# Kernel tuning notes

Hardware: AMD Instinct MI355X
Metric: run time of the kernel (lower is better)

Reference implementation:

```python
import jax, jax.numpy as jnp
import numpy as np

N_NODES = 50000
N_HYPEREDGES = 50000
E = 320000
D = 256


def _prelu(x, a):
    return jnp.where(x >= 0, x, a * x)


def _hypergraph_conv(x, hei, W, b, num_nodes, num_edges):
    # PyG HypergraphConv, use_attention=False, heads=1:
    # out = D^{-1} H B^{-1} H^T (X W^T) + b
    src = hei[0]  # node indices, [E]
    he = hei[1]   # hyperedge indices, [E]
    xw = x @ W.T  # [N, D] node transform (lin has no bias)
    ones = jnp.ones((hei.shape[1],), x.dtype)
    deg_n = jax.ops.segment_sum(ones, src, num_segments=num_nodes)   # node degree D
    deg_e = jax.ops.segment_sum(ones, he, num_segments=num_edges)    # hyperedge size B
    d_inv = jnp.where(deg_n > 0, 1.0 / deg_n, 0.0)
    b_inv = jnp.where(deg_e > 0, 1.0 / deg_e, 0.0)
    # node -> hyperedge aggregation, scaled by B^{-1}
    edge_feat = b_inv[:, None] * jax.ops.segment_sum(xw[src], he, num_segments=num_edges)  # [n_he, D]
    # hyperedge -> node aggregation, scaled by D^{-1}
    out = d_inv[:, None] * jax.ops.segment_sum(edge_feat[he], src, num_segments=num_nodes)  # [N, D]
    return out + b


def setup_inputs() -> dict:
    key = jax.random.key(0)
    ks = jax.random.split(key, 6)
    std = np.sqrt(2.0 / D)  # kaiming_normal
    x = jax.random.normal(ks[0], (N_NODES, D), dtype=jnp.float32)
    hyper_edge_index = jax.random.randint(ks[1], (2, E), 0, N_HYPEREDGES, dtype=jnp.int64)
    W1 = jax.random.normal(ks[2], (D, D), dtype=jnp.float32) * std
    b1 = jnp.zeros((D,), jnp.float32)
    W2 = jax.random.normal(ks[3], (D, D), dtype=jnp.float32) * std
    b2 = jnp.zeros((D,), jnp.float32)
    prelu_a = jnp.asarray(0.25, jnp.float32)
    return {"x": x, "W1": W1, "b1": b1, "W2": W2, "b2": b2,
            "prelu_a": prelu_a, "hyper_edge_index": hyper_edge_index}


def reference(x, W1, b1, W2, b2, prelu_a, hyper_edge_index):
    out = _hypergraph_conv(x, hyper_edge_index, W1, b1, N_NODES, N_HYPEREDGES)
    out = _prelu(out, prelu_a)
    out = _hypergraph_conv(out, hyper_edge_index, W2, b2, N_NODES, N_HYPEREDGES)
    out = out + x  # residual
    out = _prelu(out, prelu_a)
    return out
```

## Files before the change

kernel.cpp:

```cpp
#include <hip/hip_runtime.h>

#define NN    50000
#define NHE   50000
#define NEDGE 320000
#define DD    256

#define SB    1024
#define NBLK  ((NN + SB - 1) / SB)
#define CNTB  ((NEDGE / 4 + 255) / 256)

typedef float f32x4 __attribute__((ext_vector_type(4)));
typedef short short8 __attribute__((ext_vector_type(8)));

static __device__ __forceinline__ unsigned short f2b(float f) {
    union { float f; unsigned u; } c; c.f = f;
    unsigned u = c.u;
    u += 0x7fffu + ((u >> 16) & 1u);
    return (unsigned short)(u >> 16);
}
static __device__ __forceinline__ float b2f_lo(unsigned v) {
    union { unsigned u; float f; } c; c.u = v << 16; return c.f;
}
static __device__ __forceinline__ float b2f_hi(unsigned v) {
    union { unsigned u; float f; } c; c.u = v & 0xffff0000u; return c.f;
}
static __device__ __forceinline__ unsigned pack2(float a, float b) {
    return (unsigned)f2b(a) | ((unsigned)f2b(b) << 16);
}

static __device__ __forceinline__ void glds16(const unsigned short* g, unsigned short* l) {
    __builtin_amdgcn_global_load_lds((const __attribute__((address_space(1))) unsigned int*)g,
                                     (__attribute__((address_space(3))) unsigned int*)l,
                                     16, 0, 0);
}

__global__ __launch_bounds__(256) void k_count_cvt(const int* __restrict__ src,
                                                   const int* __restrict__ he,
                                                   int* __restrict__ cnt_n,
                                                   int* __restrict__ cnt_e,
                                                   int* __restrict__ rank_n,
                                                   int* __restrict__ rank_e,
                                                   const float* __restrict__ w1,
                                                   const float* __restrict__ w2,
                                                   unsigned short* __restrict__ o1,
                                                   unsigned short* __restrict__ o2) {
    int bx = blockIdx.x;
    if (bx >= CNTB) {
        int t = (bx - CNTB) * 256 + threadIdx.x;
        const int n4 = DD * DD / 4;
        const float* s = (t < n4) ? w1 : w2;
        unsigned short* d = (t < n4) ? o1 : o2;
        int i = (t < n4) ? t : t - n4;
        float4 v = ((const float4*)s)[i];
        uint2 o;
        o.x = pack2(v.x, v.y);
        o.y = pack2(v.z, v.w);
        ((uint2*)d)[i] = o;
        return;
    }
    int t  = bx * 256 + threadIdx.x;
    int e0 = t * 4;
    if (e0 >= NEDGE) return;
    int4 s = *(const int4*)(src + e0);
    int4 h = *(const int4*)(he + e0);
    int4 rn, re;
    rn.x = atomicAdd(&cnt_n[s.x], 1);
    rn.y = atomicAdd(&cnt_n[s.y], 1);
    rn.z = atomicAdd(&cnt_n[s.z], 1);
    rn.w = atomicAdd(&cnt_n[s.w], 1);
    re.x = atomicAdd(&cnt_e[h.x], 1);
    re.y = atomicAdd(&cnt_e[h.y], 1);
    re.z = atomicAdd(&cnt_e[h.z], 1);
    re.w = atomicAdd(&cnt_e[h.w], 1);
    *(int4*)(rank_n + e0) = rn;
    *(int4*)(rank_e + e0) = re;
}

__global__ __launch_bounds__(256) void k_scan_a(const int* __restrict__ cnt_n,
                                                const int* __restrict__ cnt_e,
                                                int* __restrict__ bsum) {
    int b   = blockIdx.x;
    int seg = b / NBLK, lb = b % NBLK;
    const int* cnt = seg ? cnt_e : cnt_n;
    int t = threadIdx.x;
    int idx = lb * SB + t * 4;
    int s = 0;
#pragma unroll
    for (int j = 0; j < 4; ++j)
        if (idx + j < NN) s += cnt[idx + j];
    __shared__ int red[256];
    red[t] = s;
    __syncthreads();
    for (int o = 128; o > 0; o >>= 1) {
        if (t < o) red[t] += red[t + o];
        __syncthreads();
    }
    if (t == 0) bsum[b] = red[0];
}

__global__ __launch_bounds__(256) void k_scan_c(const int* __restrict__ cnt_n,
                                                const int* __restrict__ cnt_e,
                                                const int* __restrict__ bsum,
                                                int* __restrict__ off_n,
                                                int* __restrict__ off_e) {
    int b   = blockIdx.x;
    int seg = b / NBLK, lb = b % NBLK;
    const int* cnt = seg ? cnt_e : cnt_n;
    int* off = seg ? off_e : off_n;
    int t = threadIdx.x;
    __shared__ int sb[NBLK];
    __shared__ int binfo[2];
    if (t < NBLK) sb[t] = bsum[seg * NBLK + t];
    __syncthreads();
    if (t == 0) {
        int base = 0, tot = 0;
        for (int j = 0; j < NBLK; ++j) { if (j < lb) base += sb[j]; tot += sb[j]; }
        binfo[0] = base; binfo[1] = tot;
    }
    int idx = lb * SB + t * 4;
    int v[4];
    int tsum = 0;
#pragma unroll
    for (int j = 0; j < 4; ++j) {
        v[j] = (idx + j < NN) ? cnt[idx + j] : 0;
        tsum += v[j];
    }
    __shared__ int sc[256];
    sc[t] = tsum;
    __syncthreads();
    for (int o = 1; o < 256; o <<= 1) {
        int val = (t >= o) ? sc[t - o] : 0;
        __syncthreads();
        sc[t] += val;
        __syncthreads();
    }
    int p = binfo[0] + sc[t] - tsum;
#pragma unroll
    for (int j = 0; j < 4; ++j) {
        if (idx + j < NN) off[idx + j] = p;
        p += v[j];
    }
    if (b == 0 && t == 0) off_n[NN] = binfo[1];
    if (b == NBLK && t == 0) off_e[NHE] = binfo[1];
}

__global__ __launch_bounds__(256) void k_fill(const int* __restrict__ src,
                                              const int* __restrict__ he,
                                              const int* __restrict__ off_n,
                                              const int* __restrict__ off_e,
                                              const int* __restrict__ rank_n,
                                              const int* __restrict__ rank_e,
                                              int* __restrict__ adj_n,
                                              int* __restrict__ adj_e) {
    int t  = blockIdx.x * 256 + threadIdx.x;
    int e0 = t * 4;
    if (e0 >= NEDGE) return;
    int4 s  = *(const int4*)(src + e0);
    int4 h  = *(const int4*)(he + e0);
    int4 rn = *(const int4*)(rank_n + e0);
    int4 re = *(const int4*)(rank_e + e0);
    int on0 = off_n[s.x], on1 = off_n[s.y], on2 = off_n[s.z], on3 = off_n[s.w];
    int oe0 = off_e[h.x], oe1 = off_e[h.y], oe2 = off_e[h.z], oe3 = off_e[h.w];
    adj_n[on0 + rn.x] = h.x;
    adj_n[on1 + rn.y] = h.y;
    adj_n[on2 + rn.z] = h.z;
    adj_n[on3 + rn.w] = h.w;
    adj_e[oe0 + re.x] = s.x;
    adj_e[oe1 + re.y] = s.y;
    adj_e[oe2 + re.z] = s.z;
    adj_e[oe3 + re.w] = s.w;
}

template <bool A32>
__global__ __launch_bounds__(1024) void k_gemm_bres(const void* __restrict__ Av,
                                                    const unsigned short* __restrict__ Wb,
                                                    unsigned short* __restrict__ Cb) {
    __shared__ __align__(16) unsigned short Bs[128 * 256];
    const int t    = threadIdx.x;
    const int lane = t & 63;
    const int wave = t >> 6;
    const int n0   = blockIdx.x * 128;

#pragma unroll
    for (int q = 0; q < 4; ++q) {
        int row   = q * 32 + wave * 2 + (lane >> 5);
        int chunk = lane & 31;
        glds16(Wb + (size_t)(n0 + row) * DD + ((chunk ^ (row & 7)) * 8),
               Bs + q * 8192 + wave * 512);
    }
    __syncthreads();

    const int fr = lane & 15;
    const int fq = lane >> 4;
    int chunk = blockIdx.y * 16 + wave;
    if (chunk * 16 >= NN) return;
    int m0 = chunk * 16;

    f32x4 acc[8] = {};
    short8 af[8];
    if (A32) {
        const float* p = (const float*)Av + (size_t)(m0 + fr) * DD + fq * 8;
#pragma unroll
        for (int kc = 0; kc < 8; ++kc) {
            const float* pp = p + kc * 32;
            float4 f0 = ((const float4*)pp)[0];
            float4 f1 = ((const float4*)pp)[1];
            uint4 u;
            u.x = pack2(f0.x, f0.y); u.y = pack2(f0.z, f0.w);
            u.z = pack2(f1.x, f1.y); u.w = pack2(f1.z, f1.w);
            af[kc] = *(short8*)&u;
        }
    } else {
        const unsigned short* p = (const unsigned short*)Av + (size_t)(m0 + fr) * DD + fq * 8;
#pragma unroll
        for (int kc = 0; kc < 8; ++kc)
            af[kc] = *(const short8*)(p + kc * 32);
    }

#pragma unroll
    for (int kc = 0; kc < 8; ++kc) {
#pragma unroll
        for (int nt = 0; nt < 8; ++nt) {
            int r  = nt * 16 + fr;
            int ch = (kc * 4 + fq) ^ (fr & 7);
            short8 bf = *(const short8*)(Bs + r * 256 + ch * 8);
            acc[nt] = __builtin_amdgcn_mfma_f32_16x16x32_bf16(af[kc], bf, acc[nt], 0, 0, 0);
        }
    }

#pragma unroll
    for (int nt = 0; nt < 8; ++nt)
#pragma unroll
        for (int i = 0; i < 4; ++i)
            Cb[(size_t)(m0 + fq * 4 + i) * DD + n0 + nt * 16 + fr] = f2b(acc[nt][i]);
}

static __device__ __forceinline__ void acc8(float* a, uint4 v) {
    a[0] += b2f_lo(v.x); a[1] += b2f_hi(v.x);
    a[2] += b2f_lo(v.y); a[3] += b2f_hi(v.y);
    a[4] += b2f_lo(v.z); a[5] += b2f_hi(v.z);
    a[6] += b2f_lo(v.w); a[7] += b2f_hi(v.w);
}
static __device__ __forceinline__ void gather8(const unsigned short* __restrict__ srcb,
                                               const int* __restrict__ adj,
                                               int b, int e, int sl, float* a) {
#pragma unroll
    for (int i = 0; i < 8; ++i) a[i] = 0.f;
    for (int i = b; i < e; i += 8) {
        int g0 = adj[i];
        int g[8];
        g[0] = g0;
#pragma unroll
        for (int j = 1; j < 8; ++j) g[j] = (i + j < e) ? adj[i + j] : g0;
        uint4 v[8];
#pragma unroll
        for (int j = 0; j < 8; ++j)
            v[j] = *(const uint4*)(srcb + (size_t)g[j] * DD + sl * 8);
        acc8(a, v[0]);
#pragma unroll
        for (int j = 1; j < 8; ++j)
            if (i + j < e) acc8(a, v[j]);
    }
}

__global__ __launch_bounds__(256) void k_gather_edge_b(const unsigned short* __restrict__ xw,
                                                       unsigned short* __restrict__ ef,
                                                       const int* __restrict__ off,
                                                       const int* __restrict__ adj) {
    int tid = blockIdx.x * 256 + threadIdx.x;
    int w = tid >> 5;
    int sl = tid & 31;
    if (w >= NHE) return;
    int b = off[w], e = off[w + 1];
    float a[8];
    gather8(xw, adj, b, e, sl, a);
    float sc = (e > b) ? 1.f / (float)(e - b) : 0.f;
    uint4 o;
    o.x = pack2(a[0] * sc, a[1] * sc);
    o.y = pack2(a[2] * sc, a[3] * sc);
    o.z = pack2(a[4] * sc, a[5] * sc);
    o.w = pack2(a[6] * sc, a[7] * sc);
    *(uint4*)(ef + (size_t)w * DD + sl * 8) = o;
}

__global__ __launch_bounds__(256) void k_gather_node_mid_b(const unsigned short* __restrict__ ef,
                                                           unsigned short* __restrict__ h,
                                                           const int* __restrict__ off,
                                                           const int* __restrict__ adj,
                                                           const float* __restrict__ bias,
                                                           const float* __restrict__ aP) {
    int tid = blockIdx.x * 256 + threadIdx.x;
    int w = tid >> 5;
    int sl = tid & 31;
    if (w >= NN) return;
    int b = off[w], e = off[w + 1];
    float a[8];
    gather8(ef, adj, b, e, sl, a);
    float sc = (e > b) ? 1.f / (float)(e - b) : 0.f;
    float al = *aP;
    float4 bb0 = ((const float4*)bias)[sl * 2];
    float4 bb1 = ((const float4*)bias)[sl * 2 + 1];
    float r[8];
    r[0] = a[0] * sc + bb0.x; r[1] = a[1] * sc + bb0.y;
    r[2] = a[2] * sc + bb0.z; r[3] = a[3] * sc + bb0.w;
    r[4] = a[4] * sc + bb1.x; r[5] = a[5] * sc + bb1.y;
    r[6] = a[6] * sc + bb1.z; r[7] = a[7] * sc + bb1.w;
#pragma unroll
    for (int i = 0; i < 8; ++i) r[i] = (r[i] >= 0.f) ? r[i] : al * r[i];
    uint4 o;
    o.x = pack2(r[0], r[1]);
    o.y = pack2(r[2], r[3]);
    o.z = pack2(r[4], r[5]);
    o.w = pack2(r[6], r[7]);
    *(uint4*)(h + (size_t)w * DD + sl * 8) = o;
}

__global__ __launch_bounds__(256) void k_gather_node_final_b(const unsigned short* __restrict__ ef,
                                                             const float* __restrict__ x,
                                                             float* __restrict__ out,
                                                             const int* __restrict__ off,
                                                             const int* __restrict__ adj,
                                                             const float* __restrict__ bias,
                                                             const float* __restrict__ aP) {
    int tid = blockIdx.x * 256 + threadIdx.x;
    int w = tid >> 5;
    int sl = tid & 31;
    if (w >= NN) return;
    int b = off[w], e = off[w + 1];
    float a[8];
    gather8(ef, adj, b, e, sl, a);
    float sc = (e > b) ? 1.f / (float)(e - b) : 0.f;
    float al = *aP;
    float4 bb0 = ((const float4*)bias)[sl * 2];
    float4 bb1 = ((const float4*)bias)[sl * 2 + 1];
    const float* xp = x + (size_t)w * DD + sl * 8;
    float4 xv0 = *(const float4*)xp;
    float4 xv1 = *(const float4*)(xp + 4);
    float r[8];
    r[0] = a[0] * sc + bb0.x + xv0.x; r[1] = a[1] * sc + bb0.y + xv0.y;
    r[2] = a[2] * sc + bb0.z + xv0.z; r[3] = a[3] * sc + bb0.w + xv0.w;
    r[4] = a[4] * sc + bb1.x + xv1.x; r[5] = a[5] * sc + bb1.y + xv1.y;
    r[6] = a[6] * sc + bb1.z + xv1.z; r[7] = a[7] * sc + bb1.w + xv1.w;
#pragma unroll
    for (int i = 0; i < 8; ++i) r[i] = (r[i] >= 0.f) ? r[i] : al * r[i];
    float* op = out + (size_t)w * DD + sl * 8;
    *(float4*)op = make_float4(r[0], r[1], r[2], r[3]);
    *(float4*)(op + 4) = make_float4(r[4], r[5], r[6], r[7]);
}

extern "C" void kernel_launch(void* const* d_in, const int* in_sizes, int n_in,
                              void* d_out, int out_size, void* d_ws, size_t ws_size,
                              hipStream_t stream) {
    const float* x       = (const float*)d_in[0];
    const float* W1      = (const float*)d_in[1];
    const float* b1      = (const float*)d_in[2];
    const float* W2      = (const float*)d_in[3];
    const float* b2      = (const float*)d_in[4];
    const float* prelu_a = (const float*)d_in[5];
    const int*   hei     = (const int*)d_in[6];
    const int* idx_src = hei;
    const int* idx_he  = hei + NEDGE;

    float* out = (float*)d_out;
    unsigned short* B1 = (unsigned short*)d_ws;
    unsigned short* B2 = B1 + (size_t)NN * DD;
    int* off_n  = (int*)(B2 + (size_t)NN * DD);
    int* off_e  = off_n + NN + 1;
    int* cnt_n  = off_e + NHE + 1;
    int* cnt_e  = cnt_n + NN;
    int* adj_n  = cnt_e + NHE;
    int* adj_e  = adj_n + NEDGE;
    int* rank_n = adj_e + NEDGE;
    int* rank_e = rank_n + NEDGE;
    int* bsum   = rank_e + NEDGE;
    unsigned short* w1b = (unsigned short*)d_out;
    unsigned short* w2b = w1b + DD * DD;

    const int gblocks = (NN * 32 + 255) / 256;
    dim3 ggrid(2, (NN / 16 + 15) / 16);

    hipMemsetAsync(cnt_n, 0, sizeof(int) * (NN + NHE), stream);
    k_count_cvt<<<CNTB + 128, 256, 0, stream>>>(idx_src, idx_he, cnt_n, cnt_e,
                                                rank_n, rank_e, W1, W2, w1b, w2b);
    k_scan_a<<<2 * NBLK, 256, 0, stream>>>(cnt_n, cnt_e, bsum);
    k_scan_c<<<2 * NBLK, 256, 0, stream>>>(cnt_n, cnt_e, bsum, off_n, off_e);
    k_fill<<<CNTB, 256, 0, stream>>>(idx_src, idx_he, off_n, off_e,
                                     rank_n, rank_e, adj_n, adj_e);

    k_gemm_bres<true><<<ggrid, 1024, 0, stream>>>((const void*)x, w1b, B1);
    k_gather_edge_b<<<gblocks, 256, 0, stream>>>(B1, B2, off_e, adj_e);
    k_gather_node_mid_b<<<gblocks, 256, 0, stream>>>(B2, B1, off_n, adj_n, b1, prelu_a);

    k_gemm_bres<false><<<ggrid, 1024, 0, stream>>>((const void*)B1, w2b, B2);
    k_gather_edge_b<<<gblocks, 256, 0, stream>>>(B2, B1, off_e, adj_e);
    k_gather_node_final_b<<<gblocks, 256, 0, stream>>>(B1, x, out, off_n, adj_n, b2, prelu_a);
}
```

Before: 310.5 us.

## Merge scan passes into one kernel and fuse CSR fill with first GEMM

The two-pass block scan is replaced by a single kernel in which each block recomputes its prefix by summing all preceding counts directly. The CSR adjacency fill is merged into the first GEMM launch as extra blocks, so the two independent tasks run concurrently in one grid. Together these remove two kernel launches and their serialization points. In exchange, later scan blocks do redundant prefix reads, and the fill blocks now run at 1024 threads each.

```diff
diff --git a/kernel.cpp b/kernel.cpp
--- a/kernel.cpp
+++ b/kernel.cpp
@@ -8,6 +8,7 @@
 #define SB    1024
 #define NBLK  ((NN + SB - 1) / SB)
 #define CNTB  ((NEDGE / 4 + 255) / 256)
+#define FB    ((NEDGE / 4 + 1023) / 1024)
 
 typedef float f32x4 __attribute__((ext_vector_type(4)));
 typedef short short8 __attribute__((ext_vector_type(8)));
@@ -76,18 +77,22 @@
     *(int4*)(rank_e + e0) = re;
 }
 
-__global__ __launch_bounds__(256) void k_scan_a(const int* __restrict__ cnt_n,
-                                                const int* __restrict__ cnt_e,
-                                                int* __restrict__ bsum) {
+__global__ __launch_bounds__(256) void k_scan(const int* __restrict__ cnt_n,
+                                              const int* __restrict__ cnt_e,
+                                              int* __restrict__ off_n,
+                                              int* __restrict__ off_e) {
     int b   = blockIdx.x;
     int seg = b / NBLK, lb = b % NBLK;
     const int* cnt = seg ? cnt_e : cnt_n;
+    int* off = seg ? off_e : off_n;
     int t = threadIdx.x;
-    int idx = lb * SB + t * 4;
+
+    int pre = lb * SB;
     int s = 0;
-#pragma unroll
-    for (int j = 0; j < 4; ++j)
-        if (idx + j < NN) s += cnt[idx + j];
+    for (int i = t * 4; i < pre; i += 1024) {
+        int4 c = *(const int4*)(cnt + i);
+        s += c.x + c.y + c.z + c.w;
+    }
     __shared__ int red[256];
     red[t] = s;
     __syncthreads();
@@ -95,29 +100,9 @@
         if (t < o) red[t] += red[t + o];
         __syncthreads();
     }
-    if (t == 0) bsum[b] = red[0];
-}
-
-__global__ __launch_bounds__(256) void k_scan_c(const int* __restrict__ cnt_n,
-                                                const int* __restrict__ cnt_e,
-                                                const int* __restrict__ bsum,
-                                                int* __restrict__ off_n,
-                                                int* __restrict__ off_e) {
-    int b   = blockIdx.x;
-    int seg = b / NBLK, lb = b % NBLK;
-    const int* cnt = seg ? cnt_e : cnt_n;
-    int* off = seg ? off_e : off_n;
-    int t = threadIdx.x;
-    __shared__ int sb[NBLK];
-    __shared__ int binfo[2];
-    if (t < NBLK) sb[t] = bsum[seg * NBLK + t];
-    __syncthreads();
-    if (t == 0) {
-        int base = 0, tot = 0;
-        for (int j = 0; j < NBLK; ++j) { if (j < lb) base += sb[j]; tot += sb[j]; }
-        binfo[0] = base; binfo[1] = tot;
-    }
-    int idx = lb * SB + t * 4;
+    int base = red[0];
+
+    int idx = pre + t * 4;
     int v[4];
     int tsum = 0;
 #pragma unroll
@@ -134,52 +119,25 @@
         sc[t] += val;
         __syncthreads();
     }
-    int p = binfo[0] + sc[t] - tsum;
+    int p = base + sc[t] - tsum;
 #pragma unroll
     for (int j = 0; j < 4; ++j) {
         if (idx + j < NN) off[idx + j] = p;
         p += v[j];
     }
-    if (b == 0 && t == 0) off_n[NN] = binfo[1];
-    if (b == NBLK && t == 0) off_e[NHE] = binfo[1];
-}
-
-__global__ __launch_bounds__(256) void k_fill(const int* __restrict__ src,
-                                              const int* __restrict__ he,
-                                              const int* __restrict__ off_n,
-                                              const int* __restrict__ off_e,
-                                              const int* __restrict__ rank_n,
-                                              const int* __restrict__ rank_e,
-                                              int* __restrict__ adj_n,
-                                              int* __restrict__ adj_e) {
-    int t  = blockIdx.x * 256 + threadIdx.x;
-    int e0 = t * 4;
-    if (e0 >= NEDGE) return;
-    int4 s  = *(const int4*)(src + e0);
-    int4 h  = *(const int4*)(he + e0);
-    int4 rn = *(const int4*)(rank_n + e0);
-    int4 re = *(const int4*)(rank_e + e0);
-    int on0 = off_n[s.x], on1 = off_n[s.y], on2 = off_n[s.z], on3 = off_n[s.w];
-    int oe0 = off_e[h.x], oe1 = off_e[h.y], oe2 = off_e[h.z], oe3 = off_e[h.w];
-    adj_n[on0 + rn.x] = h.x;
-    adj_n[on1 + rn.y] = h.y;
-    adj_n[on2 + rn.z] = h.z;
-    adj_n[on3 + rn.w] = h.w;
-    adj_e[oe0 + re.x] = s.x;
-    adj_e[oe1 + re.y] = s.y;
-    adj_e[oe2 + re.z] = s.z;
-    adj_e[oe3 + re.w] = s.w;
+    if (lb == NBLK - 1 && t == 255) off[NN] = base + sc[255];
 }
 
 template <bool A32>
-__global__ __launch_bounds__(1024) void k_gemm_bres(const void* __restrict__ Av,
-                                                    const unsigned short* __restrict__ Wb,
-                                                    unsigned short* __restrict__ Cb) {
+static __device__ __forceinline__ void gemm_bres_body(const void* __restrict__ Av,
+                                                      const unsigned short* __restrict__ Wb,
+                                                      unsigned short* __restrict__ Cb,
+                                                      int bid) {
     __shared__ __align__(16) unsigned short Bs[128 * 256];
     const int t    = threadIdx.x;
     const int lane = t & 63;
     const int wave = t >> 6;
-    const int n0   = blockIdx.x * 128;
+    const int n0   = (bid & 1) * 128;
 
 #pragma unroll
     for (int q = 0; q < 4; ++q) {
@@ -192,7 +150,7 @@
 
     const int fr = lane & 15;
     const int fq = lane >> 4;
-    int chunk = blockIdx.y * 16 + wave;
+    int chunk = (bid >> 1) * 16 + wave;
     if (chunk * 16 >= NN) return;
     int m0 = chunk * 16;
 
@@ -233,6 +191,47 @@
 #pragma unroll
         for (int i = 0; i < 4; ++i)
             Cb[(size_t)(m0 + fq * 4 + i) * DD + n0 + nt * 16 + fr] = f2b(acc[nt][i]);
+}
+
+__global__ __launch_bounds__(1024) void k_fill_gemm1(const int* __restrict__ src,
+                                                     const int* __restrict__ he,
+                                                     const int* __restrict__ off_n,
+                                                     const int* __restrict__ off_e,
+                                                     const int* __restrict__ rank_n,
+                                                     const int* __restrict__ rank_e,
+                                                     int* __restrict__ adj_n,
+                                                     int* __restrict__ adj_e,
+                                                     const float* __restrict__ x,
+                                                     const unsigned short* __restrict__ w1b,
+                                                     unsigned short* __restrict__ B1) {
+    int bx = blockIdx.x;
+    if (bx < FB) {
+        int t  = bx * 1024 + threadIdx.x;
+        int e0 = t * 4;
+        if (e0 >= NEDGE) return;
+        int4 s  = *(const int4*)(src + e0);
+        int4 h  = *(const int4*)(he + e0);
+        int4 rn = *(const int4*)(rank_n + e0);
+        int4 re = *(const int4*)(rank_e + e0);
+        int on0 = off_n[s.x], on1 = off_n[s.y], on2 = off_n[s.z], on3 = off_n[s.w];
+        int oe0 = off_e[h.x], oe1 = off_e[h.y], oe2 = off_e[h.z], oe3 = off_e[h.w];
+        adj_n[on0 + rn.x] = h.x;
+        adj_n[on1 + rn.y] = h.y;
+        adj_n[on2 + rn.z] = h.z;
+        adj_n[on3 + rn.w] = h.w;
+        adj_e[oe0 + re.x] = s.x;
+        adj_e[oe1 + re.y] = s.y;
+        adj_e[oe2 + re.z] = s.z;
+        adj_e[oe3 + re.w] = s.w;
+        return;
+    }
+    gemm_bres_body<true>((const void*)x, w1b, B1, bx - FB);
+}
+
+__global__ __launch_bounds__(1024) void k_gemm2(const unsigned short* __restrict__ Av,
+                                                const unsigned short* __restrict__ Wb,
+                                                unsigned short* __restrict__ Cb) {
+    gemm_bres_body<false>((const void*)Av, Wb, Cb, blockIdx.x);
 }
 
 static __device__ __forceinline__ void acc8(float* a, uint4 v) {
@@ -372,26 +371,24 @@
     int* adj_e  = adj_n + NEDGE;
     int* rank_n = adj_e + NEDGE;
     int* rank_e = rank_n + NEDGE;
-    int* bsum   = rank_e + NEDGE;
     unsigned short* w1b = (unsigned short*)d_out;
     unsigned short* w2b = w1b + DD * DD;
 
     const int gblocks = (NN * 32 + 255) / 256;
-    dim3 ggrid(2, (NN / 16 + 15) / 16);
+    const int gemmb   = 2 * ((NN / 16 + 15) / 16);
 
     hipMemsetAsync(cnt_n, 0, sizeof(int) * (NN + NHE), stream);
     k_count_cvt<<<CNTB + 128, 256, 0, stream>>>(idx_src, idx_he, cnt_n, cnt_e,
                                                 rank_n, rank_e, W1, W2, w1b, w2b);
-    k_scan_a<<<2 * NBLK, 256, 0, stream>>>(cnt_n, cnt_e, bsum);
-    k_scan_c<<<2 * NBLK, 256, 0, stream>>>(cnt_n, cnt_e, bsum, off_n, off_e);
-    k_fill<<<CNTB, 256, 0, stream>>>(idx_src, idx_he, off_n, off_e,
-                                     rank_n, rank_e, adj_n, adj_e);
-
-    k_gemm_bres<true><<<ggrid, 1024, 0, stream>>>((const void*)x, w1b, B1);
+    k_scan<<<2 * NBLK, 256, 0, stream>>>(cnt_n, cnt_e, off_n, off_e);
+
+    k_fill_gemm1<<<FB + gemmb, 1024, 0, stream>>>(idx_src, idx_he, off_n, off_e,
+                                                  rank_n, rank_e, adj_n, adj_e,
+                                                  x, w1b, B1);
     k_gather_edge_b<<<gblocks, 256, 0, stream>>>(B1, B2, off_e, adj_e);
     k_gather_node_mid_b<<<gblocks, 256, 0, stream>>>(B2, B1, off_n, adj_n, b1, prelu_a);
 
-    k_gemm_bres<false><<<ggrid, 1024, 0, stream>>>((const void*)B1, w2b, B2);
+    k_gemm2<<<gemmb, 1024, 0, stream>>>(B1, w2b, B2);
     k_gather_edge_b<<<gblocks, 256, 0, stream>>>(B2, B1, off_e, adj_e);
     k_gather_node_final_b<<<gblocks, 256, 0, stream>>>(B1, x, out, off_n, adj_n, b2, prelu_a);
 }
```

New measurement: 312.7 us. No clear change (+0.7%).
